# Performance work log

Measured on AMD Instinct MI355X. Metric: run time of the kernel, lower is better.

Reference implementation:

```python
import jax, jax.numpy as jnp
import numpy as np

# blobTverskyLoss constants
MAIN_WEIGHT = 2.0   # self.alpha -> blob_loss_dict['main_weight']
BLOB_WEIGHT = 1.0   # self.beta  -> blob_loss_dict['blob_weight']
CRIT_WEIGHT = 0.5   # per-criterion weight in criterion_dict / blob_criterion_dict
# MemoryEfficientTverskyLoss defaults (apply_nonlin=softmax dim1, batch_dice=False,
# do_bg=True, smooth=0, ddp=False); standard Tversky alpha/beta defaults assumed.
TV_ALPHA = 0.3
TV_BETA = 0.7
SMOOTH = 0.0
NUM_BLOBS = 8  # connected components per sample (fixed by construction)


def setup_inputs() -> dict:
    B, C, D, H, W = 4, 2, 64, 160, 160
    rng = np.random.default_rng(0)
    ml = np.zeros((B, D, H, W), np.int32)
    # Place 8 disjoint boxes (one per 2x2x2 octant, with >=1 voxel margin) so the
    # connected-components labeling of y=(ml>0) is exactly ml with labels 1..8.
    for b in range(B):
        lab = 1
        for i in range(2):
            for j in range(2):
                for k in range(2):
                    z0, z1 = i * D // 2, (i + 1) * D // 2
                    y0, y1 = j * H // 2, (j + 1) * H // 2
                    x0, x1 = k * W // 2, (k + 1) * W // 2
                    zs = int(rng.integers(z0 + 1, z0 + (z1 - z0) // 2))
                    ze = int(rng.integers(zs + 4, z1 - 1))
                    ys = int(rng.integers(y0 + 1, y0 + (y1 - y0) // 2))
                    ye = int(rng.integers(ys + 8, y1 - 1))
                    xs = int(rng.integers(x0 + 1, x0 + (x1 - x0) // 2))
                    xe = int(rng.integers(xs + 8, x1 - 1))
                    ml[b, zs:ze, ys:ye, xs:xe] = lab
                    lab += 1
    key = jax.random.key(0)
    x = jax.random.normal(key, (B, C, D, H, W), dtype=jnp.float32)
    return {"x": x, "multi_label": jnp.asarray(ml)}


def _tversky(logits, g):
    # logits, g: (B, C, V); Tversky per (sample, class) -> (B, C)
    p = jax.nn.softmax(logits, axis=1)
    tp = jnp.sum(p * g, axis=-1)
    fp = jnp.sum(p, axis=-1) - tp
    fn = jnp.sum(g, axis=-1) - tp
    denom = jnp.clip(tp + TV_ALPHA * fp + TV_BETA * fn + SMOOTH, 1e-8, None)
    return (tp + SMOOTH) / denom


def reference(x, multi_label):
    B, C = x.shape[0], x.shape[1]
    V = int(np.prod(x.shape[2:]))
    xf = x.reshape(B, C, V)
    ml = multi_label.reshape(B, V)

    # ---- main (compound) loss: Tversky on binary label y = (multi_label > 0) ----
    y_bin = (ml > 0).astype(jnp.int32)
    g_main = jax.nn.one_hot(y_bin, C, axis=1, dtype=xf.dtype)      # (B,C,V)
    main_loss = -jnp.mean(_tversky(xf, g_main))                    # -tversky.mean()

    # ---- blob loss: per connected component, mask out OTHER blobs' logits ----
    def blob_tv(k):
        lab = k + 1
        keep = ((ml == 0) | (ml == lab)).astype(xf.dtype)          # (B,V) mask
        g_k = jax.nn.one_hot((ml == lab).astype(jnp.int32), C, axis=1, dtype=xf.dtype)
        return _tversky(xf * keep[:, None, :], g_k)                # (B,C)

    tv_blob = jax.lax.map(blob_tv, jnp.arange(NUM_BLOBS))          # (K,B,C)
    # per blob call: loss = -mean over classes, weighted by CRIT_WEIGHT;
    # mean over blobs per element, then mean over batch elements
    blob_loss = jnp.mean(CRIT_WEIGHT * (-jnp.mean(tv_blob, axis=-1)))

    loss = MAIN_WEIGHT * (CRIT_WEIGHT * main_loss) + BLOB_WEIGHT * blob_loss
    return loss
```

## Files before the change

kernel.cpp:

```cpp
#include <hip/hip_runtime.h>

#define BATCH 4
#define NCLS 2
#define VOX 1638400
#define VOX4 (VOX / 4)
#define BLOCKS_X 512
#define THREADS 256
#define NACC 19

__global__ __launch_bounds__(THREADS) void blob_reduce_kernel(
    const float* __restrict__ x, const int* __restrict__ ml,
    float* __restrict__ partials)
{
    const int b = blockIdx.y;
    const float4* __restrict__ x0v = (const float4*)(x + (size_t)b * NCLS * VOX);
    const float4* __restrict__ x1v = (const float4*)(x + (size_t)b * NCLS * VOX + VOX);
    const int4*   __restrict__ mlv = (const int4*)(ml + (size_t)b * VOX);

    float acc[NACC];
#pragma unroll
    for (int j = 0; j < NACC; ++j) acc[j] = 0.f;

    const int stride = BLOCKS_X * THREADS;
    for (int i = blockIdx.x * THREADS + threadIdx.x; i < VOX4; i += stride) {
        float4 a0 = x0v[i];
        float4 a1 = x1v[i];
        int4   m  = mlv[i];
        float xs0[4] = {a0.x, a0.y, a0.z, a0.w};
        float xs1[4] = {a1.x, a1.y, a1.z, a1.w};
        int   ls[4]  = {m.x, m.y, m.z, m.w};
#pragma unroll
        for (int e = 0; e < 4; ++e) {
            float p0 = 1.0f / (1.0f + __expf(xs1[e] - xs0[e]));
            int L = ls[e];
            acc[0] += p0;
            bool z = (L == 0);
            acc[1] += z ? p0 : 0.f;
            acc[2] += z ? 1.f : 0.f;
#pragma unroll
            for (int l = 0; l < 8; ++l) {
                bool eq = (L == l + 1);
                acc[3 + l]  += eq ? p0 : 0.f;
                acc[11 + l] += eq ? 1.f : 0.f;
            }
        }
    }

    __shared__ float red[4][NACC];
    const int lane = threadIdx.x & 63;
    const int wave = threadIdx.x >> 6;
#pragma unroll
    for (int j = 0; j < NACC; ++j) {
        float v = acc[j];
        for (int off = 32; off > 0; off >>= 1) v += __shfl_down(v, off, 64);
        if (lane == 0) red[wave][j] = v;
    }
    __syncthreads();
    if (threadIdx.x < NACC) {
        float s = red[0][threadIdx.x] + red[1][threadIdx.x] +
                  red[2][threadIdx.x] + red[3][threadIdx.x];
        partials[((size_t)threadIdx.x * BATCH + b) * BLOCKS_X + blockIdx.x] = s;
    }
}

__global__ __launch_bounds__(512) void blob_finalize_kernel(
    const float* __restrict__ partials, float* __restrict__ out)
{
    __shared__ double totals[NACC * BATCH];
    const int lane = threadIdx.x & 63;
    const int wave = threadIdx.x >> 6;

    for (int p = wave; p < NACC * BATCH; p += 8) {
        double s = 0.0;
#pragma unroll
        for (int i = 0; i < BLOCKS_X / 64; ++i)
            s += (double)partials[(size_t)p * BLOCKS_X + lane + i * 64];
        for (int off = 32; off > 0; off >>= 1) s += __shfl_down(s, off, 64);
        if (lane == 0) totals[p] = s;
    }
    __syncthreads();

    if (threadIdx.x == 0) {
        const double Vd = (double)VOX;
        const double TA = 0.3, TB = 0.7;
        double sum_main = 0.0, sum_blob = 0.0;
        for (int b = 0; b < BATCH; ++b) {
            const double S0 = totals[0 * BATCH + b];
            const double A  = totals[1 * BATCH + b];
            const double n0 = totals[2 * BATCH + b];
            {
                double tp = A, fp = S0 - A, fn = n0 - A;
                sum_main += tp / fmax(tp + TA * fp + TB * fn, 1e-8);
            }
            {
                double tp = (Vd - n0) - (S0 - A);
                double fp = (Vd - S0) - tp;
                double fn = (Vd - n0) - tp;
                sum_main += tp / fmax(tp + TA * fp + TB * fn, 1e-8);
            }
            for (int k = 0; k < 8; ++k) {
                const double P0 = totals[(3 + k) * BATCH + b];
                const double Nl = totals[(11 + k) * BATCH + b];
                const double P1 = Nl - P0;
                const double m  = Vd - n0 - Nl;
                {
                    double tp = A + 0.5 * m;
                    double fp = P0;
                    double fn = (Vd - Nl) - tp;
                    sum_blob += tp / fmax(tp + TA * fp + TB * fn, 1e-8);
                }
                {
                    double tp = P1;
                    double fp = (n0 - A) + 0.5 * m;
                    double fn = P0;
                    sum_blob += tp / fmax(tp + TA * fp + TB * fn, 1e-8);
                }
            }
        }
        out[0] = (float)(-(sum_main / 8.0 + sum_blob / 128.0));
    }
}

extern "C" void kernel_launch(void* const* d_in, const int* in_sizes, int n_in,
                              void* d_out, int out_size, void* d_ws, size_t ws_size,
                              hipStream_t stream) {
    const float* x  = (const float*)d_in[0];
    const int*   ml = (const int*)d_in[1];
    float* out      = (float*)d_out;
    float* partials = (float*)d_ws;

    dim3 grid(BLOCKS_X, BATCH);
    blob_reduce_kernel<<<grid, THREADS, 0, stream>>>(x, ml, partials);
    blob_finalize_kernel<<<1, 512, 0, stream>>>(partials, out);
}
```

Baseline: 113.8 us.

## Fuse finalize into reduce via last-block counter, skip empty-label work

Merges the two kernels into one, where the last block to finish (found with an atomic counter) performs the final reduction. The per-element accumulator work becomes wave-uniform: a ballot skips label handling when a wave holds only background, and a wave-wide OR of present labels limits the work to labels that actually occur. The accumulator count drops from 19 to 17 by deriving S0 and n0 algebraically, and the reciprocal uses a fast hardware rcp. In exchange it adds a memset launch, threadfence and atomic overhead, and slightly less precise arithmetic.

```diff
diff --git a/kernel.cpp b/kernel.cpp
--- a/kernel.cpp
+++ b/kernel.cpp
@@ -1,57 +1,84 @@
 #include <hip/hip_runtime.h>
 
 #define BATCH 4
-#define NCLS 2
 #define VOX 1638400
 #define VOX4 (VOX / 4)
 #define BLOCKS_X 512
 #define THREADS 256
-#define NACC 19
+#define NACC 17
+#define NTOT (NACC * BATCH)
+#define TOTAL_BLOCKS (BLOCKS_X * BATCH)
 
-__global__ __launch_bounds__(THREADS) void blob_reduce_kernel(
+__device__ __forceinline__ float p0_of(float d) {
+    float e = __expf(d);
+#if __has_builtin(__builtin_amdgcn_rcpf)
+    return __builtin_amdgcn_rcpf(1.0f + e);
+#else
+    return 1.0f / (1.0f + e);
+#endif
+}
+
+__global__ __launch_bounds__(THREADS) void blob_fused_kernel(
     const float* __restrict__ x, const int* __restrict__ ml,
-    float* __restrict__ partials)
+    float* __restrict__ partials, unsigned int* __restrict__ counter,
+    float* __restrict__ out)
 {
-    const int b = blockIdx.y;
-    const float4* __restrict__ x0v = (const float4*)(x + (size_t)b * NCLS * VOX);
-    const float4* __restrict__ x1v = (const float4*)(x + (size_t)b * NCLS * VOX + VOX);
+    const int b  = blockIdx.y;
+    const int bx = blockIdx.x;
+    const float4* __restrict__ x0v = (const float4*)(x + (size_t)b * 2 * VOX);
+    const float4* __restrict__ x1v = (const float4*)(x + (size_t)b * 2 * VOX + VOX);
     const int4*   __restrict__ mlv = (const int4*)(ml + (size_t)b * VOX);
 
-    float acc[NACC];
+    float accA = 0.f;
+    float accP[8], accN[8];
 #pragma unroll
-    for (int j = 0; j < NACC; ++j) acc[j] = 0.f;
+    for (int k = 0; k < 8; ++k) { accP[k] = 0.f; accN[k] = 0.f; }
 
     const int stride = BLOCKS_X * THREADS;
-    for (int i = blockIdx.x * THREADS + threadIdx.x; i < VOX4; i += stride) {
+    for (int i = bx * THREADS + threadIdx.x; i < VOX4; i += stride) {
         float4 a0 = x0v[i];
         float4 a1 = x1v[i];
         int4   m  = mlv[i];
-        float xs0[4] = {a0.x, a0.y, a0.z, a0.w};
-        float xs1[4] = {a1.x, a1.y, a1.z, a1.w};
-        int   ls[4]  = {m.x, m.y, m.z, m.w};
+        float p0 = p0_of(a1.x - a0.x);
+        float p1 = p0_of(a1.y - a0.y);
+        float p2 = p0_of(a1.z - a0.z);
+        float p3 = p0_of(a1.w - a0.w);
+        int orl = m.x | m.y | m.z | m.w;
+        if (__ballot(orl != 0) == 0ull) {
+            accA += (p0 + p1) + (p2 + p3);
+        } else {
+            unsigned pres = (1u << m.x) | (1u << m.y) | (1u << m.z) | (1u << m.w);
 #pragma unroll
-        for (int e = 0; e < 4; ++e) {
-            float p0 = 1.0f / (1.0f + __expf(xs1[e] - xs0[e]));
-            int L = ls[e];
-            acc[0] += p0;
-            bool z = (L == 0);
-            acc[1] += z ? p0 : 0.f;
-            acc[2] += z ? 1.f : 0.f;
+            for (int off = 1; off < 64; off <<= 1) pres |= __shfl_xor((int)pres, off, 64);
+            pres = (unsigned)__builtin_amdgcn_readfirstlane((int)pres);
+
+            accA += (m.x == 0 ? p0 : 0.f) + (m.y == 0 ? p1 : 0.f) +
+                    (m.z == 0 ? p2 : 0.f) + (m.w == 0 ? p3 : 0.f);
 #pragma unroll
-            for (int l = 0; l < 8; ++l) {
-                bool eq = (L == l + 1);
-                acc[3 + l]  += eq ? p0 : 0.f;
-                acc[11 + l] += eq ? 1.f : 0.f;
+            for (int l = 1; l <= 8; ++l) {
+                if (pres & (1u << l)) {
+                    float ps = (m.x == l ? p0 : 0.f) + (m.y == l ? p1 : 0.f) +
+                               (m.z == l ? p2 : 0.f) + (m.w == l ? p3 : 0.f);
+                    float ns = (m.x == l ? 1.f : 0.f) + (m.y == l ? 1.f : 0.f) +
+                               (m.z == l ? 1.f : 0.f) + (m.w == l ? 1.f : 0.f);
+                    accP[l - 1] += ps;
+                    accN[l - 1] += ns;
+                }
             }
         }
     }
+
+    float accs[NACC];
+    accs[0] = accA;
+#pragma unroll
+    for (int k = 0; k < 8; ++k) { accs[1 + k] = accP[k]; accs[9 + k] = accN[k]; }
 
     __shared__ float red[4][NACC];
     const int lane = threadIdx.x & 63;
     const int wave = threadIdx.x >> 6;
 #pragma unroll
     for (int j = 0; j < NACC; ++j) {
-        float v = acc[j];
+        float v = accs[j];
         for (int off = 32; off > 0; off >>= 1) v += __shfl_down(v, off, 64);
         if (lane == 0) red[wave][j] = v;
     }
@@ -59,65 +86,70 @@
     if (threadIdx.x < NACC) {
         float s = red[0][threadIdx.x] + red[1][threadIdx.x] +
                   red[2][threadIdx.x] + red[3][threadIdx.x];
-        partials[((size_t)threadIdx.x * BATCH + b) * BLOCKS_X + blockIdx.x] = s;
+        partials[((size_t)threadIdx.x * BATCH + b) * BLOCKS_X + bx] = s;
     }
-}
 
-__global__ __launch_bounds__(512) void blob_finalize_kernel(
-    const float* __restrict__ partials, float* __restrict__ out)
-{
-    __shared__ double totals[NACC * BATCH];
-    const int lane = threadIdx.x & 63;
-    const int wave = threadIdx.x >> 6;
-
-    for (int p = wave; p < NACC * BATCH; p += 8) {
-        double s = 0.0;
-#pragma unroll
-        for (int i = 0; i < BLOCKS_X / 64; ++i)
-            s += (double)partials[(size_t)p * BLOCKS_X + lane + i * 64];
-        for (int off = 32; off > 0; off >>= 1) s += __shfl_down(s, off, 64);
-        if (lane == 0) totals[p] = s;
+    __shared__ unsigned amLast;
+    __threadfence();
+    if (threadIdx.x == 0) {
+        unsigned old = atomicAdd(counter, 1u);
+        amLast = (old == TOTAL_BLOCKS - 1) ? 1u : 0u;
     }
     __syncthreads();
-
-    if (threadIdx.x == 0) {
-        const double Vd = (double)VOX;
-        const double TA = 0.3, TB = 0.7;
-        double sum_main = 0.0, sum_blob = 0.0;
-        for (int b = 0; b < BATCH; ++b) {
-            const double S0 = totals[0 * BATCH + b];
-            const double A  = totals[1 * BATCH + b];
-            const double n0 = totals[2 * BATCH + b];
-            {
-                double tp = A, fp = S0 - A, fn = n0 - A;
-                sum_main += tp / fmax(tp + TA * fp + TB * fn, 1e-8);
+    if (amLast) {
+        __threadfence();
+        __shared__ double totals[NTOT];
+        for (int p = wave; p < NTOT; p += 4) {
+            double s = 0.0;
+#pragma unroll
+            for (int i = 0; i < BLOCKS_X / 64; ++i) {
+                float f = __hip_atomic_load(&partials[(size_t)p * BLOCKS_X + lane + i * 64],
+                                            __ATOMIC_RELAXED, __HIP_MEMORY_SCOPE_AGENT);
+                s += (double)f;
             }
-            {
-                double tp = (Vd - n0) - (S0 - A);
-                double fp = (Vd - S0) - tp;
-                double fn = (Vd - n0) - tp;
-                sum_main += tp / fmax(tp + TA * fp + TB * fn, 1e-8);
-            }
-            for (int k = 0; k < 8; ++k) {
-                const double P0 = totals[(3 + k) * BATCH + b];
-                const double Nl = totals[(11 + k) * BATCH + b];
-                const double P1 = Nl - P0;
-                const double m  = Vd - n0 - Nl;
+            for (int off = 32; off > 0; off >>= 1) s += __shfl_down(s, off, 64);
+            if (lane == 0) totals[p] = s;
+        }
+        __syncthreads();
+        if (threadIdx.x == 0) {
+            const double Vd = (double)VOX;
+            const double TA = 0.3, TB = 0.7;
+            double sum_main = 0.0, sum_blob = 0.0;
+            for (int bb = 0; bb < BATCH; ++bb) {
+                double A = totals[0 * BATCH + bb];
+                double P[8], N[8], SP = 0.0, SN = 0.0;
+                for (int k = 0; k < 8; ++k) {
+                    P[k] = totals[(1 + k) * BATCH + bb];
+                    N[k] = totals[(9 + k) * BATCH + bb];
+                    SP += P[k]; SN += N[k];
+                }
+                double n0 = Vd - SN;
                 {
-                    double tp = A + 0.5 * m;
-                    double fp = P0;
-                    double fn = (Vd - Nl) - tp;
-                    sum_blob += tp / fmax(tp + TA * fp + TB * fn, 1e-8);
+                    double tp = A, fp = SP, fn = n0 - A;
+                    sum_main += tp / fmax(tp + TA * fp + TB * fn, 1e-8);
                 }
                 {
-                    double tp = P1;
-                    double fp = (n0 - A) + 0.5 * m;
-                    double fn = P0;
-                    sum_blob += tp / fmax(tp + TA * fp + TB * fn, 1e-8);
+                    double tp = SN - SP, fp = n0 - A, fn = SP;
+                    sum_main += tp / fmax(tp + TA * fp + TB * fn, 1e-8);
+                }
+                for (int k = 0; k < 8; ++k) {
+                    double mo = SN - N[k];
+                    {
+                        double tp = A + 0.5 * mo;
+                        double fp = P[k];
+                        double fn = (Vd - N[k]) - tp;
+                        sum_blob += tp / fmax(tp + TA * fp + TB * fn, 1e-8);
+                    }
+                    {
+                        double tp = N[k] - P[k];
+                        double fp = (n0 - A) + 0.5 * mo;
+                        double fn = P[k];
+                        sum_blob += tp / fmax(tp + TA * fp + TB * fn, 1e-8);
+                    }
                 }
             }
+            out[0] = (float)(-(sum_main / 8.0 + sum_blob / 128.0));
         }
-        out[0] = (float)(-(sum_main / 8.0 + sum_blob / 128.0));
     }
 }
 
@@ -128,8 +160,10 @@
     const int*   ml = (const int*)d_in[1];
     float* out      = (float*)d_out;
     float* partials = (float*)d_ws;
+    unsigned int* counter =
+        (unsigned int*)((char*)d_ws + (size_t)NTOT * BLOCKS_X * sizeof(float));
 
+    hipMemsetAsync(counter, 0, sizeof(unsigned int), stream);
     dim3 grid(BLOCKS_X, BATCH);
-    blob_reduce_kernel<<<grid, THREADS, 0, stream>>>(x, ml, partials);
-    blob_finalize_kernel<<<1, 512, 0, stream>>>(partials, out);
+    blob_fused_kernel<<<grid, THREADS, 0, stream>>>(x, ml, partials, counter, out);
 }
```

New measurement: 275.3 us. 2.42x slower.
